# Kernel tuning notes

Measured on AMD Instinct MI355X. Metric: run time of the kernel, lower is better.

Reference implementation:

```python
import jax, jax.numpy as jnp
import numpy as np

N_NODES = 256
IN_FEATURES = 4096
OUT_FEATURES = 7
LAYERS = 4
WIRES = 8                      # ceil(log2(n_nodes))
DIM = 2 ** WIRES               # state-vector length = 256
P2 = WIRES * (WIRES - 1) // 2  # 28 controlled gates per block
N_W = 6 * WIRES + 3 * P2       # 132 weights per layer (matches weight_shape)
CPLX = jnp.complex64
# op2_all_layers ordering: gaps 1..w-1, then j
PAIRS = [(j, j + gap) for gap in range(1, WIRES) for j in range(WIRES - gap)]


def _ry(t):
    c, s = jnp.cos(t / 2), jnp.sin(t / 2)
    return jnp.stack([jnp.stack([c, -s]), jnp.stack([s, c])]).astype(CPLX)


def _rx(t):
    c = jnp.cos(t / 2).astype(CPLX)
    s = (-1j * jnp.sin(t / 2)).astype(CPLX)
    return jnp.stack([jnp.stack([c, s]), jnp.stack([s, c])])


def _rz(t):
    z = jnp.zeros((), CPLX)
    return jnp.stack([jnp.stack([jnp.exp(-0.5j * t).astype(CPLX), z]),
                      jnp.stack([z, jnp.exp(0.5j * t).astype(CPLX)])])


# Constant-angle gates (the source passes the integer weight index as the
# controlled-rotation angle, so these are compile-time numpy constants).
def _ry_np(a):
    c, s = np.cos(a / 2), np.sin(a / 2)
    return np.array([[c, -s], [s, c]], np.complex64)


def _rx_np(a):
    c, s = np.cos(a / 2), np.sin(a / 2)
    return np.array([[c, -1j * s], [-1j * s, c]], np.complex64)


def _rz_np(a):
    return np.diag([np.exp(-0.5j * a), np.exp(0.5j * a)]).astype(np.complex64)


def apply_1q(state, M, q):
    # state: [B] + [2]*WIRES; wire q lives on axis q+1 (wire 0 = MSB, PennyLane order)
    s = jnp.moveaxis(state, q + 1, -1)
    s = jnp.einsum('...b,ab->...a', s, M)
    return jnp.moveaxis(s, -1, q + 1)


def apply_c1q(state, M, c, t):
    # controlled gate: apply M on target wire t in the control==1 subspace
    s = jnp.moveaxis(state, (c + 1, t + 1), (-2, -1))
    s1 = jnp.einsum('...b,ab->...a', s[..., 1, :], M)
    s = jnp.stack([s[..., 0, :], s1], axis=-2)
    return jnp.moveaxis(s, (-2, -1), (c + 1, t + 1))


def q_layer(state, wv):
    # Faithful port of the source q_layer, including the quirk that the
    # CRY/CRX/CRZ angles are the integer running weight index (constants).
    wi = 0
    for q in range(WIRES):
        state = apply_1q(state, _ry(wv[wi + q]), q)
    wi += WIRES
    for i, (c, t) in enumerate(PAIRS):
        state = apply_c1q(state, _ry_np(float(wi + i)), c, t)
    wi += P2
    for q in range(WIRES):
        state = apply_1q(state, _ry(wv[wi + q]), q)
    wi += WIRES
    for q in range(WIRES):
        state = apply_1q(state, _rx(wv[wi + q]), q)
    wi += WIRES
    for i, (c, t) in enumerate(PAIRS):
        state = apply_c1q(state, _rx_np(float(wi + i)), c, t)
    wi += P2
    for q in range(WIRES):
        state = apply_1q(state, _rx(wv[wi + q]), q)
    wi += WIRES
    for q in range(WIRES):
        state = apply_1q(state, _rz(wv[wi + q]), q)
    wi += WIRES
    for i, (c, t) in enumerate(PAIRS):
        state = apply_c1q(state, _rz_np(float(wi + i)), c, t)
    wi += P2
    for q in range(WIRES):
        state = apply_1q(state, _rz(wv[wi + q]), q)
    return state


def circuit(samples, qweights):
    # samples: [B, N_NODES] real -> AmplitudeEmbedding(pad_with=0, normalize=True)
    B = samples.shape[0]
    v = samples
    if DIM > N_NODES:
        v = jnp.pad(v, ((0, 0), (0, DIM - N_NODES)))
    v = v / jnp.linalg.norm(v, axis=1, keepdims=True)
    state = v.astype(CPLX).reshape((B,) + (2,) * WIRES)
    layer = jax.checkpoint(q_layer)  # bounds residual memory under AD
    for l in range(LAYERS):
        state = layer(state, qweights[l])
    p = state.real ** 2 + state.imag ** 2  # probabilities, [B] + [2]*WIRES
    zs = []
    for q in range(WIRES):
        axes = tuple(a for a in range(1, WIRES + 1) if a != q + 1)
        m = p.sum(axis=axes)            # [B, 2]
        zs.append(m[:, 0] - m[:, 1])    # <Z_q> = P(0) - P(1)
    return jnp.stack(zs, axis=1)        # [B, WIRES]


def setup_inputs() -> dict:
    key = jax.random.key(0)
    k1, k2, k3, k4 = jax.random.split(key, 4)
    x = jax.random.normal(k1, (N_NODES, IN_FEATURES), jnp.float32)
    qweights = jax.random.uniform(k2, (LAYERS, N_W), jnp.float32, 0.0, 2.0 * np.pi)
    fc_w = jax.random.normal(k3, (OUT_FEATURES, WIRES), jnp.float32) / np.sqrt(WIRES)
    fc_b = jax.random.normal(k4, (OUT_FEATURES,), jnp.float32) / np.sqrt(WIRES)
    return {"x": x, "qweights": qweights, "fc_w": fc_w, "fc_b": fc_b}


def reference(x, qweights, fc_w, fc_b):
    z = circuit(x.T, qweights)      # [IN_FEATURES, WIRES]
    return z @ fc_w.T + fc_b        # [IN_FEATURES, OUT_FEATURES]
```

## Files before the change

### kernel.cpp

```cpp
#include <hip/hip_runtime.h>
#include <math.h>


namespace {

constexpr int NSAMP = 4096;
constexpr int NW_L  = 132;

constexpr double PI_D   = 3.14159265358979323846264338327950288;
constexpr double TWO_PI = 6.28318530717958647692528676655900577;

constexpr double red_pm_pi(double x) {
  double k = x / TWO_PI;
  long long ki = (long long)k;
  double r = x - (double)ki * TWO_PI;
  if (r > PI_D)  r -= TWO_PI;
  if (r < -PI_D) r += TWO_PI;
  return r;
}
constexpr double csin(double x) {
  double r = red_pm_pi(x), r2 = r * r, term = r, sum = r;
  for (int n = 1; n <= 13; ++n) { term *= -r2 / (double)((2*n)*(2*n+1)); sum += term; }
  return sum;
}
constexpr double ccos(double x) {
  double r = red_pm_pi(x), r2 = r * r, term = 1.0, sum = 1.0;
  for (int n = 1; n <= 13; ++n) { term *= -r2 / (double)((2*n-1)*(2*n)); sum += term; }
  return sum;
}

constexpr int PC[28] = {0,1,2,3,4,5,6, 0,1,2,3,4,5, 0,1,2,3,4, 0,1,2,3, 0,1,2, 0,1, 0};
constexpr int PT[28] = {1,2,3,4,5,6,7, 2,3,4,5,6,7, 3,4,5,6,7, 4,5,6,7, 5,6,7, 6,7, 7};

struct Tbl28 { float c[28]; float s[28]; };
constexpr Tbl28 mk_tbl(int base) {
  Tbl28 t{};
  for (int i = 0; i < 28; ++i) {
    double a = 0.5 * (double)(base + i);
    t.c[i] = (float)ccos(a);
    t.s[i] = (float)csin(a);
  }
  return t;
}
constexpr Tbl28 T_CRY = mk_tbl(8);
constexpr Tbl28 T_CRX = mk_tbl(52);

struct DTbl { float v[512]; };
constexpr DTbl mk_dcrz() {
  DTbl t{};
  for (int s = 0; s < 256; ++s) {
    double psi = 0.0;
    for (int i = 0; i < 28; ++i) {
      const int pc = 7 - PC[i], pt = 7 - PT[i];
      if ((s >> pc) & 1) {
        const double half = 0.5 * (double)(96 + i);
        psi += ((s >> pt) & 1) ? half : -half;
      }
    }
    t.v[2*s]   = (float)ccos(psi);
    t.v[2*s+1] = (float)csin(psi);
  }
  return t;
}
__device__ constexpr DTbl D_CRZ = mk_dcrz();

__device__ __forceinline__ float shx1(float v, int p) {
  if (p == 0) {
    int r = __builtin_amdgcn_update_dpp((int)__float_as_uint(v), (int)__float_as_uint(v),
                                        0xB1, 0xF, 0xF, true);
    return __uint_as_float((unsigned)r);
  }
  if (p == 1) {
    int r = __builtin_amdgcn_update_dpp((int)__float_as_uint(v), (int)__float_as_uint(v),
                                        0x4E, 0xF, 0xF, true);
    return __uint_as_float((unsigned)r);
  }
  if (p == 2) return __uint_as_float((unsigned)__builtin_amdgcn_ds_swizzle(
                      (int)__float_as_uint(v), 0x101F));
  if (p == 3) return __uint_as_float((unsigned)__builtin_amdgcn_ds_swizzle(
                      (int)__float_as_uint(v), 0x201F));
  if (p == 4) return __uint_as_float((unsigned)__builtin_amdgcn_ds_swizzle(
                      (int)__float_as_uint(v), 0x401F));
  return __shfl_xor(v, 32, 64);
}

__device__ __forceinline__ void gen_lane(float& ar, float& ai, int s, int p,
                                         float m00r, float m00i, float m01r, float m01i) {
  const int b = (s >> p) & 1;
  const float dr = m00r;
  const float di = b ? -m00i : m00i;
  const float g  = b ? -m01r : m01r;
  const float hh = m01i;
  const float pr = shx1(ar, p);
  const float pi = shx1(ai, p);
  const float mr = ar, mi = ai;
  ar = dr*mr - di*mi + g*pr - hh*pi;
  ai = dr*mi + di*mr + g*pi + hh*pr;
}
__device__ __forceinline__ void gen_xw(float& ar, float& ai, int s, int p,
                                       float m00r, float m00i, float m01r, float m01i,
                                       float2* xbuf) {
  xbuf[s] = make_float2(ar, ai);
  __syncthreads();
  const float2 pt = xbuf[s ^ (1 << p)];
  __syncthreads();
  const int b = (s >> p) & 1;
  const float dr = m00r;
  const float di = b ? -m00i : m00i;
  const float g  = b ? -m01r : m01r;
  const float hh = m01i;
  const float mr = ar, mi = ai;
  ar = dr*mr - di*mi + g*pt.x - hh*pt.y;
  ai = dr*mi + di*mr + g*pt.y + hh*pt.x;
}
__device__ __forceinline__ void cry_lane(float& ar, float& ai, int s, int pc, int pt,
                                         float cc, float sc) {
  const int ctrl = (s >> pc) & 1;
  const float ce = ctrl ? cc : 1.0f;
  float se = ((s >> pt) & 1) ? sc : -sc;
  se = ctrl ? se : 0.0f;
  const float pr = shx1(ar, pt);
  const float pi = shx1(ai, pt);
  ar = ce*ar + se*pr;
  ai = ce*ai + se*pi;
}
__device__ __forceinline__ void cry_xw(float& ar, float& ai, int s, int pc, int pt,
                                       float cc, float sc, float2* xbuf) {
  xbuf[s] = make_float2(ar, ai);
  __syncthreads();
  const float2 p = xbuf[s ^ (1 << pt)];
  __syncthreads();
  const int ctrl = (s >> pc) & 1;
  const float ce = ctrl ? cc : 1.0f;
  float se = ((s >> pt) & 1) ? sc : -sc;
  se = ctrl ? se : 0.0f;
  ar = ce*ar + se*p.x;
  ai = ce*ai + se*p.y;
}
__device__ __forceinline__ void crx_lane(float& ar, float& ai, int s, int pc, int pt,
                                         float cc, float sc) {
  const int ctrl = (s >> pc) & 1;
  const float ce = ctrl ? cc : 1.0f;
  const float se = ctrl ? sc : 0.0f;
  const float pr = shx1(ar, pt);
  const float pi = shx1(ai, pt);
  ar = ce*ar + se*pi;
  ai = ce*ai - se*pr;
}
__device__ __forceinline__ void crx_xw(float& ar, float& ai, int s, int pc, int pt,
                                       float cc, float sc, float2* xbuf) {
  xbuf[s] = make_float2(ar, ai);
  __syncthreads();
  const float2 p = xbuf[s ^ (1 << pt)];
  __syncthreads();
  const int ctrl = (s >> pc) & 1;
  const float ce = ctrl ? cc : 1.0f;
  const float se = ctrl ? sc : 0.0f;
  ar = ce*ar + se*p.y;
  ai = ce*ai - se*p.x;
}

__device__ __forceinline__ unsigned short f2bf(float f) {
  unsigned int u = __float_as_uint(f);
  u = (u + 0x7FFFu + ((u >> 16) & 1u)) >> 16;
  return (unsigned short)u;
}

typedef __attribute__((ext_vector_type(8))) short bf16x8;
typedef __attribute__((ext_vector_type(4))) float f32x4;

}

__global__ __launch_bounds__(256) void build_rows4w(const float* __restrict__ qw,
                                                    unsigned short* __restrict__ U1bf,
                                                    unsigned short* __restrict__ W2bf) {
  __shared__ float4 sM[48];
  __shared__ float2 xbuf[256];
  const int tid = threadIdx.x;
  const int h   = blockIdx.x >> 8;
  const int o   = blockIdx.x & 255;
  const int s   = tid;

  if (tid < 48) {
    const int lp  = tid / 24;
    const int rem = tid - lp * 24;
    const int j   = rem >> 3;
    const int q   = rem & 7;
    const int l   = 2 * h + lp;
    float a, bb;
    if (j == 0) {
      a  = qw[l * NW_L + q];
      bb = (l > 0) ? qw[(l - 1) * NW_L + 124 + q] : 0.f;
    } else if (j == 1) {
      a  = qw[l * NW_L + 44 + q];
      bb = qw[l * NW_L + 36 + q];
    } else {
      a  = (l < 3) ? qw[l * NW_L + 88 + q] : 0.f;
      bb = qw[l * NW_L + 80 + q];
    }
    float sa, ca, sb, cb;
    __sincosf(0.5f * a,  &sa, &ca);
    __sincosf(0.5f * bb, &sb, &cb);
    float4 m;
    if (j == 0)      m = make_float4(ca*cb, -ca*sb, -sa*cb, -sa*sb);
    else if (j == 1) m = make_float4(ca*cb, -sa*sb, -ca*sb, -sa*cb);
    else             m = make_float4(ca*cb, -sa*cb, -sb*sa, -sb*ca);
    sM[tid] = m;
  }

  float ar = (s == o) ? 1.f : 0.f;
  float ai = 0.f;
  const float dzr =  D_CRZ.v[2*s];
  const float dzi = -D_CRZ.v[2*s+1];
  __syncthreads();

#pragma unroll 1
  for (int lp = 1; lp >= 0; --lp) {
    const int l    = 2 * h + lp;
    const int base = lp * 24;
    if (l < 3) {
      const float mr = ar, mi = ai;
      ar = mr*dzr - mi*dzi;
      ai = mr*dzi + mi*dzr;
    }
#pragma unroll
    for (int q = 0; q < 8; ++q) {
      float4 m = sM[base + 16 + q];
      if (q == 0)      gen_xw(ar, ai, s, 7, m.x, -m.y, -m.z, -m.w, xbuf);
      else if (q == 1) gen_xw(ar, ai, s, 6, m.x, -m.y, -m.z, -m.w, xbuf);
      else             gen_lane(ar, ai, s, 7 - q, m.x, -m.y, -m.z, -m.w);
    }
#pragma unroll
    for (int i = 27; i >= 0; --i) {
      const int pc = 7 - PC[i], pt = 7 - PT[i];
      const float cc = T_CRX.c[i], sc = -T_CRX.s[i];
      if (pt == 6) crx_xw(ar, ai, s, pc, pt, cc, sc, xbuf);
      else         crx_lane(ar, ai, s, pc, pt, cc, sc);
    }
#pragma unroll
    for (int q = 0; q < 8; ++q) {
      float4 m = sM[base + 8 + q];
      if (q == 0)      gen_xw(ar, ai, s, 7, m.x, -m.y, -m.z, -m.w, xbuf);
      else if (q == 1) gen_xw(ar, ai, s, 6, m.x, -m.y, -m.z, -m.w, xbuf);
      else             gen_lane(ar, ai, s, 7 - q, m.x, -m.y, -m.z, -m.w);
    }
#pragma unroll
    for (int i = 27; i >= 0; --i) {
      const int pc = 7 - PC[i], pt = 7 - PT[i];
      const float cc = T_CRY.c[i], sc = -T_CRY.s[i];
      if (pt == 6) cry_xw(ar, ai, s, pc, pt, cc, sc, xbuf);
      else         cry_lane(ar, ai, s, pc, pt, cc, sc);
    }
#pragma unroll
    for (int q = 0; q < 8; ++q) {
      float4 m = sM[base + q];
      if (q == 0)      gen_xw(ar, ai, s, 7, m.x, -m.y, -m.z, -m.w, xbuf);
      else if (q == 1) gen_xw(ar, ai, s, 6, m.x, -m.y, -m.z, -m.w, xbuf);
      else             gen_lane(ar, ai, s, 7 - q, m.x, -m.y, -m.z, -m.w);
    }
  }

  if (h == 0) {
    U1bf[(size_t)o * 256 + s]         = f2bf(ar);
    U1bf[(size_t)(o + 256) * 256 + s] = f2bf(-ai);
  } else {
    U1bf += 0;
    W2bf[(size_t)o * 512 + s]               = f2bf(ar);
    W2bf[(size_t)o * 512 + 256 + s]         = f2bf(ai);
    W2bf[(size_t)(o + 256) * 512 + s]       = f2bf(-ai);
    W2bf[(size_t)(o + 256) * 512 + 256 + s] = f2bf(ar);
  }
}

__global__ __launch_bounds__(1024) void eval_chain(const float* __restrict__ x,
                                                   const unsigned short* __restrict__ U1bf,
                                                   const unsigned short* __restrict__ W2bf,
                                                   const float* __restrict__ fcw,
                                                   const float* __restrict__ fcb,
                                                   float* __restrict__ out) {
  __shared__ unsigned short Xs[16 * 264];
  __shared__ unsigned short Ys[16 * 520];
  __shared__ float Zp[16][16][9];
  __shared__ float Zf[16][9];
  const int tid  = threadIdx.x;
  const int lane = tid & 63;
  const int w    = tid >> 6;
  const int colbase = blockIdx.x * 16;

  {
    const int k  = tid >> 2;
    const int c4 = (tid & 3) * 4;
    const float4 v = *(const float4*)(x + (size_t)k * NSAMP + colbase + c4);
    Xs[(c4 + 0) * 264 + k] = f2bf(v.x);
    Xs[(c4 + 1) * 264 + k] = f2bf(v.y);
    Xs[(c4 + 2) * 264 + k] = f2bf(v.z);
    Xs[(c4 + 3) * 264 + k] = f2bf(v.w);
  }
  __syncthreads();

  const int quad = lane >> 4;
  const int n    = lane & 15;
  const int rowb = w * 32;

  {
    f32x4 a1[2];
    a1[0] = (f32x4){0.f, 0.f, 0.f, 0.f};
    a1[1] = (f32x4){0.f, 0.f, 0.f, 0.f};
#pragma unroll
    for (int kt = 0; kt < 8; ++kt) {
      const bf16x8 bfrag = *(const bf16x8*)&Xs[n * 264 + kt * 32 + quad * 8];
#pragma unroll
      for (int rt = 0; rt < 2; ++rt) {
        const int row = rowb + rt * 16 + n;
        const bf16x8 afrag = *(const bf16x8*)(U1bf + (size_t)row * 256 + kt * 32 + quad * 8);
        a1[rt] = __builtin_amdgcn_mfma_f32_16x16x32_bf16(afrag, bfrag, a1[rt], 0, 0, 0);
      }
    }
#pragma unroll
    for (int rt = 0; rt < 2; ++rt) {
      unsigned short p4[4];
#pragma unroll
      for (int reg = 0; reg < 4; ++reg) p4[reg] = f2bf(a1[rt][reg]);
      *(uint2*)&Ys[n * 520 + rowb + rt * 16 + quad * 4] = *(const uint2*)p4;
    }
  }
  __syncthreads();

  f32x4 acc[2];
  acc[0] = (f32x4){0.f, 0.f, 0.f, 0.f};
  acc[1] = (f32x4){0.f, 0.f, 0.f, 0.f};
#pragma unroll
  for (int kt = 0; kt < 16; ++kt) {
    const bf16x8 bfrag = *(const bf16x8*)&Ys[n * 520 + kt * 32 + quad * 8];
#pragma unroll
    for (int rt = 0; rt < 2; ++rt) {
      const int row = rowb + rt * 16 + n;
      const bf16x8 afrag = *(const bf16x8*)(W2bf + (size_t)row * 512 + kt * 32 + quad * 8);
      acc[rt] = __builtin_amdgcn_mfma_f32_16x16x32_bf16(afrag, bfrag, acc[rt], 0, 0, 0);
    }
  }

  float za[9];
#pragma unroll
  for (int i = 0; i < 9; ++i) za[i] = 0.f;
  const float m4 = (lane & 32) ? -1.f : 1.f;
  const float m5 = (lane & 16) ? -1.f : 1.f;
#pragma unroll
  for (int rt = 0; rt < 2; ++rt) {
#pragma unroll
    for (int reg = 0; reg < 4; ++reg) {
      const float v = acc[rt][reg];
      const float p = v * v;
      za[0] += p;
      za[1] += (w & 4)   ? -p : p;
      za[2] += (w & 2)   ? -p : p;
      za[3] += (w & 1)   ? -p : p;
      za[4] += rt        ? -p : p;
      za[5] = fmaf(m4, p, za[5]);
      za[6] = fmaf(m5, p, za[6]);
      za[7] += (reg & 2) ? -p : p;
      za[8] += (reg & 1) ? -p : p;
    }
  }
#pragma unroll
  for (int off = 16; off <= 32; off <<= 1) {
#pragma unroll
    for (int i = 0; i < 9; ++i) za[i] += __shfl_xor(za[i], off, 64);
  }
  if (lane < 16) {
#pragma unroll
    for (int i = 0; i < 9; ++i) Zp[w][lane][i] = za[i];
  }
  __syncthreads();

  if (tid < 144) {
    const int col = tid / 9, q = tid - col * 9;
    float z = 0.f;
#pragma unroll
    for (int ww = 0; ww < 16; ++ww) z += Zp[ww][col][q];
    Zf[col][q] = z;
  }
  __syncthreads();

  if (tid < 112) {
    const int col = tid / 7, oo = tid - col * 7;
    const float inv = 1.f / Zf[col][0];
    float v = fcb[oo];
#pragma unroll
    for (int q = 0; q < 8; ++q)
      v = fmaf(fcw[oo * 8 + q], Zf[col][1 + q] * inv, v);
    out[(size_t)(colbase + col) * 7 + oo] = v;
  }
}

extern "C" void kernel_launch(void* const* d_in, const int* in_sizes, int n_in,
                              void* d_out, int out_size, void* d_ws, size_t ws_size,
                              hipStream_t stream) {
  const float* x   = (const float*)d_in[0];
  const float* qw  = (const float*)d_in[1];
  const float* fcw = (const float*)d_in[2];
  const float* fcb = (const float*)d_in[3];
  float* out = (float*)d_out;

  unsigned short* U1bf = (unsigned short*)d_ws;
  unsigned short* W2bf = U1bf + (size_t)512 * 256;

  hipLaunchKernelGGL(build_rows4w, dim3(512), dim3(256),  0, stream, qw, U1bf, W2bf);
  hipLaunchKernelGGL(eval_chain,   dim3(256), dim3(1024), 0, stream,
                     x, U1bf, W2bf, fcw, fcb, out);
}
```

Measured before the change: 94.60 us.

## Double-buffer shuffle exchange and store compact U2 instead of expanded real block matrix

The gate-build kernel now alternates between two shared exchange buffers, which removes the second barrier in each cross-wave exchange. The second-stage matrix is stored in compact form (real rows and negated imaginary rows, 256 wide) rather than as a 512x512 real block matrix. The evaluation kernel rebuilds the complex product by reading the two halves of the intermediate with offset selection and a sign-flip XOR, which halves the weight data read from global memory and the write volume in the build kernel. The risk is added index and sign logic, and possible mistakes in the sign convention.

New measurement: 93.38 us. No clear change (-1.3%).

```diff
diff --git a/kernel.cpp b/kernel.cpp
--- a/kernel.cpp
+++ b/kernel.cpp
@@ -99,11 +99,10 @@
 }
 __device__ __forceinline__ void gen_xw(float& ar, float& ai, int s, int p,
                                        float m00r, float m00i, float m01r, float m01i,
-                                       float2* xbuf) {
-  xbuf[s] = make_float2(ar, ai);
-  __syncthreads();
-  const float2 pt = xbuf[s ^ (1 << p)];
-  __syncthreads();
+                                       float2* buf) {
+  buf[s] = make_float2(ar, ai);
+  __syncthreads();
+  const float2 pt = buf[s ^ (1 << p)];
   const int b = (s >> p) & 1;
   const float dr = m00r;
   const float di = b ? -m00i : m00i;
@@ -125,11 +124,10 @@
   ai = ce*ai + se*pi;
 }
 __device__ __forceinline__ void cry_xw(float& ar, float& ai, int s, int pc, int pt,
-                                       float cc, float sc, float2* xbuf) {
-  xbuf[s] = make_float2(ar, ai);
-  __syncthreads();
-  const float2 p = xbuf[s ^ (1 << pt)];
-  __syncthreads();
+                                       float cc, float sc, float2* buf) {
+  buf[s] = make_float2(ar, ai);
+  __syncthreads();
+  const float2 p = buf[s ^ (1 << pt)];
   const int ctrl = (s >> pc) & 1;
   const float ce = ctrl ? cc : 1.0f;
   float se = ((s >> pt) & 1) ? sc : -sc;
@@ -148,11 +146,10 @@
   ai = ce*ai - se*pr;
 }
 __device__ __forceinline__ void crx_xw(float& ar, float& ai, int s, int pc, int pt,
-                                       float cc, float sc, float2* xbuf) {
-  xbuf[s] = make_float2(ar, ai);
-  __syncthreads();
-  const float2 p = xbuf[s ^ (1 << pt)];
-  __syncthreads();
+                                       float cc, float sc, float2* buf) {
+  buf[s] = make_float2(ar, ai);
+  __syncthreads();
+  const float2 p = buf[s ^ (1 << pt)];
   const int ctrl = (s >> pc) & 1;
   const float ce = ctrl ? cc : 1.0f;
   const float se = ctrl ? sc : 0.0f;
@@ -168,14 +165,15 @@
 
 typedef __attribute__((ext_vector_type(8))) short bf16x8;
 typedef __attribute__((ext_vector_type(4))) float f32x4;
+typedef __attribute__((ext_vector_type(4))) unsigned int u32x4;
 
 }
 
 __global__ __launch_bounds__(256) void build_rows4w(const float* __restrict__ qw,
                                                     unsigned short* __restrict__ U1bf,
-                                                    unsigned short* __restrict__ W2bf) {
+                                                    unsigned short* __restrict__ U2bf) {
   __shared__ float4 sM[48];
-  __shared__ float2 xbuf[256];
+  __shared__ float2 xb[2][256];
   const int tid = threadIdx.x;
   const int h   = blockIdx.x >> 8;
   const int o   = blockIdx.x & 255;
@@ -214,6 +212,7 @@
   const float dzi = -D_CRZ.v[2*s+1];
   __syncthreads();
 
+  int pb = 0;
 #pragma unroll 1
   for (int lp = 1; lp >= 0; --lp) {
     const int l    = 2 * h + lp;
@@ -226,58 +225,48 @@
 #pragma unroll
     for (int q = 0; q < 8; ++q) {
       float4 m = sM[base + 16 + q];
-      if (q == 0)      gen_xw(ar, ai, s, 7, m.x, -m.y, -m.z, -m.w, xbuf);
-      else if (q == 1) gen_xw(ar, ai, s, 6, m.x, -m.y, -m.z, -m.w, xbuf);
-      else             gen_lane(ar, ai, s, 7 - q, m.x, -m.y, -m.z, -m.w);
+      if (q <= 1) { gen_xw(ar, ai, s, 7 - q, m.x, -m.y, -m.z, -m.w, xb[pb]); pb ^= 1; }
+      else        gen_lane(ar, ai, s, 7 - q, m.x, -m.y, -m.z, -m.w);
     }
 #pragma unroll
     for (int i = 27; i >= 0; --i) {
       const int pc = 7 - PC[i], pt = 7 - PT[i];
       const float cc = T_CRX.c[i], sc = -T_CRX.s[i];
-      if (pt == 6) crx_xw(ar, ai, s, pc, pt, cc, sc, xbuf);
+      if (pt == 6) { crx_xw(ar, ai, s, pc, pt, cc, sc, xb[pb]); pb ^= 1; }
       else         crx_lane(ar, ai, s, pc, pt, cc, sc);
     }
 #pragma unroll
     for (int q = 0; q < 8; ++q) {
       float4 m = sM[base + 8 + q];
-      if (q == 0)      gen_xw(ar, ai, s, 7, m.x, -m.y, -m.z, -m.w, xbuf);
-      else if (q == 1) gen_xw(ar, ai, s, 6, m.x, -m.y, -m.z, -m.w, xbuf);
-      else             gen_lane(ar, ai, s, 7 - q, m.x, -m.y, -m.z, -m.w);
+      if (q <= 1) { gen_xw(ar, ai, s, 7 - q, m.x, -m.y, -m.z, -m.w, xb[pb]); pb ^= 1; }
+      else        gen_lane(ar, ai, s, 7 - q, m.x, -m.y, -m.z, -m.w);
     }
 #pragma unroll
     for (int i = 27; i >= 0; --i) {
       const int pc = 7 - PC[i], pt = 7 - PT[i];
       const float cc = T_CRY.c[i], sc = -T_CRY.s[i];
-      if (pt == 6) cry_xw(ar, ai, s, pc, pt, cc, sc, xbuf);
+      if (pt == 6) { cry_xw(ar, ai, s, pc, pt, cc, sc, xb[pb]); pb ^= 1; }
       else         cry_lane(ar, ai, s, pc, pt, cc, sc);
     }
 #pragma unroll
     for (int q = 0; q < 8; ++q) {
       float4 m = sM[base + q];
-      if (q == 0)      gen_xw(ar, ai, s, 7, m.x, -m.y, -m.z, -m.w, xbuf);
-      else if (q == 1) gen_xw(ar, ai, s, 6, m.x, -m.y, -m.z, -m.w, xbuf);
-      else             gen_lane(ar, ai, s, 7 - q, m.x, -m.y, -m.z, -m.w);
-    }
-  }
-
-  if (h == 0) {
-    U1bf[(size_t)o * 256 + s]         = f2bf(ar);
-    U1bf[(size_t)(o + 256) * 256 + s] = f2bf(-ai);
-  } else {
-    U1bf += 0;
-    W2bf[(size_t)o * 512 + s]               = f2bf(ar);
-    W2bf[(size_t)o * 512 + 256 + s]         = f2bf(ai);
-    W2bf[(size_t)(o + 256) * 512 + s]       = f2bf(-ai);
-    W2bf[(size_t)(o + 256) * 512 + 256 + s] = f2bf(ar);
-  }
-}
-
-__global__ __launch_bounds__(1024) void eval_chain(const float* __restrict__ x,
-                                                   const unsigned short* __restrict__ U1bf,
-                                                   const unsigned short* __restrict__ W2bf,
-                                                   const float* __restrict__ fcw,
-                                                   const float* __restrict__ fcb,
-                                                   float* __restrict__ out) {
+      if (q <= 1) { gen_xw(ar, ai, s, 7 - q, m.x, -m.y, -m.z, -m.w, xb[pb]); pb ^= 1; }
+      else        gen_lane(ar, ai, s, 7 - q, m.x, -m.y, -m.z, -m.w);
+    }
+  }
+
+  unsigned short* Ub = h ? U2bf : U1bf;
+  Ub[(size_t)o * 256 + s]         = f2bf(ar);
+  Ub[(size_t)(o + 256) * 256 + s] = f2bf(-ai);
+}
+
+__global__ __launch_bounds__(1024) void eval_chain2(const float* __restrict__ x,
+                                                    const unsigned short* __restrict__ U1bf,
+                                                    const unsigned short* __restrict__ U2bf,
+                                                    const float* __restrict__ fcw,
+                                                    const float* __restrict__ fcb,
+                                                    float* __restrict__ out) {
   __shared__ unsigned short Xs[16 * 264];
   __shared__ unsigned short Ys[16 * 520];
   __shared__ float Zp[16][16][9];
@@ -326,17 +315,33 @@
   }
   __syncthreads();
 
+  const int o0 = (rowb & 255);
+  const int offA = (w < 8) ? 0 : 256;
+  const int offB = (w < 8) ? 256 : 0;
+  const unsigned negmask = (w < 8) ? 0x80008000u : 0u;
   f32x4 acc[2];
   acc[0] = (f32x4){0.f, 0.f, 0.f, 0.f};
   acc[1] = (f32x4){0.f, 0.f, 0.f, 0.f};
 #pragma unroll
-  for (int kt = 0; kt < 16; ++kt) {
-    const bf16x8 bfrag = *(const bf16x8*)&Ys[n * 520 + kt * 32 + quad * 8];
+  for (int kt = 0; kt < 8; ++kt) {
+    const bf16x8 bf1 = *(const bf16x8*)&Ys[n * 520 + offA + kt * 32 + quad * 8];
 #pragma unroll
     for (int rt = 0; rt < 2; ++rt) {
-      const int row = rowb + rt * 16 + n;
-      const bf16x8 afrag = *(const bf16x8*)(W2bf + (size_t)row * 512 + kt * 32 + quad * 8);
-      acc[rt] = __builtin_amdgcn_mfma_f32_16x16x32_bf16(afrag, bfrag, acc[rt], 0, 0, 0);
+      const int row = o0 + rt * 16 + n;
+      const bf16x8 afrag = *(const bf16x8*)(U2bf + (size_t)row * 256 + kt * 32 + quad * 8);
+      acc[rt] = __builtin_amdgcn_mfma_f32_16x16x32_bf16(afrag, bf1, acc[rt], 0, 0, 0);
+    }
+  }
+#pragma unroll
+  for (int kt = 0; kt < 8; ++kt) {
+    union { bf16x8 h; u32x4 u; } t;
+    t.h = *(const bf16x8*)&Ys[n * 520 + offB + kt * 32 + quad * 8];
+    t.u ^= (u32x4){negmask, negmask, negmask, negmask};
+#pragma unroll
+    for (int rt = 0; rt < 2; ++rt) {
+      const int row = 256 + o0 + rt * 16 + n;
+      const bf16x8 afrag = *(const bf16x8*)(U2bf + (size_t)row * 256 + kt * 32 + quad * 8);
+      acc[rt] = __builtin_amdgcn_mfma_f32_16x16x32_bf16(afrag, t.h, acc[rt], 0, 0, 0);
     }
   }
 
@@ -403,9 +408,9 @@
   float* out = (float*)d_out;
 
   unsigned short* U1bf = (unsigned short*)d_ws;
-  unsigned short* W2bf = U1bf + (size_t)512 * 256;
-
-  hipLaunchKernelGGL(build_rows4w, dim3(512), dim3(256),  0, stream, qw, U1bf, W2bf);
-  hipLaunchKernelGGL(eval_chain,   dim3(256), dim3(1024), 0, stream,
-                     x, U1bf, W2bf, fcw, fcb, out);
-}
+  unsigned short* U2bf = U1bf + (size_t)512 * 256;
+
+  hipLaunchKernelGGL(build_rows4w, dim3(512), dim3(256),  0, stream, qw, U1bf, U2bf);
+  hipLaunchKernelGGL(eval_chain2,  dim3(256), dim3(1024), 0, stream,
+                     x, U1bf, U2bf, fcw, fcb, out);
+}
```
